# Kernel tuning notes

Measured on AMD Instinct MI355X. Metric: run time of the kernel, lower is better.

Reference implementation:

```python
import jax, jax.numpy as jnp
import numpy as np

N, E = 131072, 64
REL_SIZES = {0: (262144, 1), 1: (524288, 2), 2: (393216, 3)}  # idx_len, arity


def _mish(x):
    return x * jnp.tanh(jax.nn.softplus(x))


def _mlp(x, rw, rb, ow, ob):
    # torch MLP: output(input + mish(residual(input)))
    return (x + _mish(x @ rw + rb)) @ ow + ob


def setup_inputs() -> dict:
    key = jax.random.key(0)
    ks = jax.random.split(key, 16)

    def lin(k, fi, fo):
        k1, k2 = jax.random.split(k)
        lim = 1.0 / np.sqrt(fi)
        w = jax.random.uniform(k1, (fi, fo), jnp.float32, -lim, lim)
        b = jax.random.uniform(k2, (fo,), jnp.float32, -lim, lim)
        return w, b

    inp = {"obj_emb": jax.random.normal(ks[0], (N, E), jnp.float32)}
    for r in range(3):
        L, _ = REL_SIZES[r]
        inp[f"rel{r}_idx"] = jax.random.randint(ks[1 + r], (L,), 0, N, jnp.int64)
    for r in range(3):
        _, a = REL_SIZES[r]
        d = a * E
        w, b = lin(ks[4 + 2 * r], d, d)
        inp[f"r{r}_res_w"], inp[f"r{r}_res_b"] = w, b
        w, b = lin(ks[5 + 2 * r], d, d)
        inp[f"r{r}_out_w"], inp[f"r{r}_out_b"] = w, b
    w, b = lin(ks[10], 2 * E, 2 * E)
    inp["upd_res_w"], inp["upd_res_b"] = w, b
    w, b = lin(ks[11], 2 * E, E)
    inp["upd_out_w"], inp["upd_out_b"] = w, b
    return inp


def _forward(obj_emb, idxs, rel_params, upd_params):
    n, e = obj_emb.shape
    outs = []
    for (idx, a), (rw, rb, ow, ob) in zip(idxs, rel_params):
        g = obj_emb[idx].reshape(-1, a * e)          # gather -> [T, a*E]
        outs.append((idx, _mlp(g, rw, rb, ow, ob).reshape(-1, e)))
    # First scatter_reduce_('amax', include_self=False): positions written by
    # relation 0 ignore the initial 0; all other positions keep/compete with 0.
    written0 = jnp.zeros((n,), bool).at[idxs[0][0]].set(True)
    m = jnp.broadcast_to(jnp.where(written0[:, None], -jnp.inf, 0.0).astype(obj_emb.dtype), (n, e))
    for idx, out in outs:
        m = m.at[idx].max(out)
    m = jax.lax.stop_gradient(m)
    s = jnp.full((n, e), 1e-16, obj_emb.dtype)
    for idx, out in outs:
        s = s.at[idx].add(jnp.exp(12.0 * (out - m[idx])))
    max_msg = jnp.log(s) / 12.0 + m
    return _mlp(jnp.concatenate([max_msg, obj_emb], axis=1), *upd_params)


def reference(obj_emb, rel0_idx, rel1_idx, rel2_idx,
              r0_res_w, r0_res_b, r0_out_w, r0_out_b,
              r1_res_w, r1_res_b, r1_out_w, r1_out_b,
              r2_res_w, r2_res_b, r2_out_w, r2_out_b,
              upd_res_w, upd_res_b, upd_out_w, upd_out_b):
    idxs = [(rel0_idx, 1), (rel1_idx, 2), (rel2_idx, 3)]
    rel_params = [
        (r0_res_w, r0_res_b, r0_out_w, r0_out_b),
        (r1_res_w, r1_res_b, r1_out_w, r1_out_b),
        (r2_res_w, r2_res_b, r2_out_w, r2_out_b),
    ]
    return _forward(obj_emb, idxs, rel_params,
                    (upd_res_w, upd_res_b, upd_out_w, upd_out_b))
```

## Files before the change

kernel.cpp:

```cpp
#include <hip/hip_runtime.h>
#include <stdint.h>

typedef unsigned short u16;
typedef __bf16 bf16x8 __attribute__((ext_vector_type(8)));
typedef float floatx4 __attribute__((ext_vector_type(4)));

#define N_OBJ    131072
#define L0R      262144
#define L1R      524288
#define L2R      393216
#define TOTI     (L0R + L1R + L2R)


__device__ __forceinline__ float bf2f(u16 u) {
  union { uint32_t i; float f; } v; v.i = ((uint32_t)u) << 16; return v.f;
}
__device__ __forceinline__ u16 f2bf(float f) {
  union { float f; uint32_t i; } v; v.f = f;
  uint32_t r = (v.i + 0x7FFFu + ((v.i >> 16) & 1u)) >> 16;
  return (u16)r;
}
__device__ __forceinline__ uint4 pack8(const float* sp) {
  float4 f0 = *(const float4*)(sp);
  float4 f1 = *(const float4*)(sp + 4);
  uint4 v;
  v.x = (uint32_t)f2bf(f0.x) | ((uint32_t)f2bf(f0.y) << 16);
  v.y = (uint32_t)f2bf(f0.z) | ((uint32_t)f2bf(f0.w) << 16);
  v.z = (uint32_t)f2bf(f1.x) | ((uint32_t)f2bf(f1.y) << 16);
  v.w = (uint32_t)f2bf(f1.z) | ((uint32_t)f2bf(f1.w) << 16);
  return v;
}
__device__ __forceinline__ float mish_f(float x) {
  float t = __expf(fminf(x, 30.f));
  float u = 1.f + t; u = u * u;
  return x * (u - 1.f) / (u + 1.f);
}

__global__ __launch_bounds__(256) void norm_kernel(
    const int* __restrict__ r0, const int* __restrict__ r1,
    const int* __restrict__ r2, int* __restrict__ n)
{
  int g = blockIdx.x * 256 + (int)threadIdx.x;
  const int* src; int off;
  if (g < L0R)              { src = r0; off = g; }
  else if (g < L0R + L1R)   { src = r1; off = g - L0R; }
  else                      { src = r2; off = g - L0R - L1R; }
  int lane = (int)threadIdx.x & 63;
  int probe = src[2 * lane + 1];
  bool i64 = (__ballot(probe == 0) == ~0ull);
  n[g] = i64 ? src[2 * off] : src[off];
}

__global__ __launch_bounds__(256) void prep_kernel(
    const float* w0, const float* w1, const float* w2, const float* w3,
    const float* w4, const float* w5, const float* w6, const float* w7,
    u16* __restrict__ wt)
{
  int b = blockIdx.x;
  const float* srcs[8] = {w0, w1, w2, w3, w4, w5, w6, w7};
  const int fi[8]   = {64, 64, 128, 128, 192, 192, 128, 128};
  const int fo[8]   = {64, 64, 128, 128, 192, 192, 128, 64};
  const int boff[9] = {0, 16, 32, 96, 160, 304, 448, 512, 544};
  const int woff[8] = {0, 4096, 8192, 24576, 40960, 77824, 114688, 131072};
  int m = 0;
  #pragma unroll
  for (int j = 0; j < 8; ++j) if (b >= boff[j + 1]) m = j + 1;
  int e = (b - boff[m]) * 256 + (int)threadIdx.x;
  int k = e / fo[m];
  int n = e - k * fo[m];
  wt[woff[m] + n * fi[m] + k] = f2bf(srcs[m][e]);
}

__global__ __launch_bounds__(256) void flag_kernel(
    const int* __restrict__ idx0, unsigned char* __restrict__ flag)
{
  int g = blockIdx.x * 256 + (int)threadIdx.x;
  flag[idx0[g]] = 1;
}

template<int D, int NTOUT>
__device__ __forceinline__ void matmul_phase(
    const u16* __restrict__ wtsrc, u16* w_lds,
    const bf16x8 (&af)[D / 32], floatx4 (&acc)[D / 16],
    int tid, int q, int i)
{
  constexpr int PITCH = D + 8;
  #pragma unroll
  for (int t = 0; t < NTOUT; ++t) acc[t] = (floatx4)0.f;
  #pragma unroll
  for (int ch = 0; ch < NTOUT / 4; ++ch) {
    __syncthreads();
    for (int c = tid; c < 64 * (D / 8); c += 256) {
      int nr = c / (D / 8), p = c - nr * (D / 8);
      *(uint4*)(&w_lds[nr * PITCH + p * 8]) =
          *(const uint4*)(wtsrc + (size_t)(ch * 64 + nr) * D + p * 8);
    }
    __syncthreads();
    #pragma unroll
    for (int k = 0; k < D / 32; ++k) {
      #pragma unroll
      for (int nt = 0; nt < 4; ++nt) {
        bf16x8 bf = *(const bf16x8*)(&w_lds[(nt * 16 + i) * PITCH + k * 32 + q * 8]);
        acc[ch * 4 + nt] =
            __builtin_amdgcn_mfma_f32_16x16x32_bf16(af[k], bf, acc[ch * 4 + nt], 0, 0, 0);
      }
    }
  }
}

template<int D, int DOUT, int MODE>
__global__ __launch_bounds__(256, (D >= 192) ? 3 : 4) void mlp_kernel(
    const float* __restrict__ srcE, const u16* __restrict__ srcM,
    const int* __restrict__ idx,
    const u16* __restrict__ rwt, const float* __restrict__ rb,
    const u16* __restrict__ owt, const float* __restrict__ ob,
    float* __restrict__ dstF, float* __restrict__ dstS)
{
  constexpr int A = D / 64;
  constexpr int PITCH = D + 8;
  constexpr int NT1 = D / 16;
  constexpr int NT2 = DOUT / 16;
  constexpr int KI = D / 32;
  __shared__ alignas(16) u16 g_lds[64 * PITCH];
  __shared__ alignas(16) u16 w_lds[64 * PITCH];
  __shared__ float b1_lds[D];
  __shared__ float b2_lds[DOUT];
  __shared__ int i_lds[64 * A];

  const int tid = threadIdx.x;
  const int wave = tid >> 6;
  const int lane = tid & 63;
  const int q = lane >> 4;
  const int i = lane & 15;
  const int t0 = blockIdx.x * 64;

  for (int c = tid; c < D; c += 256) b1_lds[c] = rb[c];
  for (int c = tid; c < DOUT; c += 256) b2_lds[c] = ob[c];
  if (MODE == 0 && tid < 64 * A) i_lds[tid] = idx[t0 * A + tid];

  for (int c = tid; c < 64 * A * 8; c += 256) {
    int e = c >> 3, p = c & 7;
    int r = e / A, sl = e - r * A;
    uint4 val;
    if (MODE == 0) {
      int obj = idx[(t0 + r) * A + sl];
      val = pack8(srcE + (size_t)obj * 64 + p * 8);
    } else {
      if (sl == 0) val = *(const uint4*)(srcM + (size_t)(t0 + r) * 64 + p * 8);
      else         val = pack8(srcE + (size_t)(t0 + r) * 64 + p * 8);
    }
    *(uint4*)(&g_lds[r * PITCH + sl * 64 + p * 8]) = val;
  }
  __syncthreads();

  floatx4 acc[NT1];
  bf16x8 af[KI];

  #pragma unroll
  for (int k = 0; k < KI; ++k)
    af[k] = *(const bf16x8*)(&g_lds[(wave * 16 + i) * PITCH + k * 32 + q * 8]);
  matmul_phase<D, NT1>(rwt, w_lds, af, acc, tid, q, i);

  #pragma unroll
  for (int t = 0; t < NT1; ++t) {
    #pragma unroll
    for (int r = 0; r < 4; ++r) {
      int row = wave * 16 + q * 4 + r;
      int col = t * 16 + i;
      float h = acc[t][r] + b1_lds[col];
      float g = bf2f(g_lds[row * PITCH + col]);
      g_lds[row * PITCH + col] = f2bf(g + mish_f(h));
    }
  }

  #pragma unroll
  for (int k = 0; k < KI; ++k)
    af[k] = *(const bf16x8*)(&g_lds[(wave * 16 + i) * PITCH + k * 32 + q * 8]);
  matmul_phase<D, NT2>(owt, w_lds, af, acc, tid, q, i);

  #pragma unroll
  for (int t = 0; t < NT2; ++t) {
    #pragma unroll
    for (int r = 0; r < 4; ++r) {
      int row = wave * 16 + q * 4 + r;
      int col = t * 16 + i;
      float y = acc[t][r] + b2_lds[col];
      if (MODE == 0) {
        int slot = col >> 6, cc = col & 63;
        int obj = i_lds[row * A + slot];
        atomicAdd(&dstS[(size_t)obj * 64 + cc], __expf(fminf(12.f * y, 82.f)));
      } else {
        dstF[(size_t)(t0 + row) * 64 + col] = y;
      }
    }
  }
}

__global__ __launch_bounds__(256) void final_kernel(
    const float* __restrict__ s, const unsigned char* __restrict__ flag,
    u16* __restrict__ maxmsg)
{
  int tid = (int)threadIdx.x;
  int o = blockIdx.x * 64 + (tid >> 2);
  int c0 = (tid & 3) * 16;
  float add = flag[o] ? 1e-37f : 1e-16f;
  const float* sp = s + (size_t)o * 64 + c0;
  u16* mp = maxmsg + (size_t)o * 64 + c0;
  u16 tmp[16];
  #pragma unroll
  for (int j = 0; j < 16; ++j)
    tmp[j] = f2bf(__logf(sp[j] + add) * (1.f / 12.f));
  *(uint4*)(mp)     = *(uint4*)(tmp);
  *(uint4*)(mp + 8) = *(uint4*)(tmp + 8);
}

extern "C" void kernel_launch(void* const* d_in, const int* in_sizes, int n_in,
                              void* d_out, int out_size, void* d_ws, size_t ws_size,
                              hipStream_t stream)
{
  (void)in_sizes; (void)n_in; (void)out_size; (void)ws_size;
  const float* obj_emb = (const float*)d_in[0];
  const float* r0rb = (const float*)d_in[5];
  const float* r0ob = (const float*)d_in[7];
  const float* r1rb = (const float*)d_in[9];
  const float* r1ob = (const float*)d_in[11];
  const float* r2rb = (const float*)d_in[13];
  const float* r2ob = (const float*)d_in[15];
  const float* urb  = (const float*)d_in[17];
  const float* uob  = (const float*)d_in[19];

  char* ws = (char*)d_ws;
  float* s           = (float*)(ws);
  u16* wt            = (u16*)(ws + 33554432ull);
  unsigned char* flg = (unsigned char*)(ws + 33832960ull);
  u16* maxmsg        = (u16*)(ws + 33964032ull);
  int* nidx          = (int*)(ws + 50741248ull);
  float* out         = (float*)d_out;

  hipMemsetAsync(s, 0, 64ull * N_OBJ * 4ull, stream);
  hipMemsetAsync(flg, 0, N_OBJ, stream);

  norm_kernel<<<TOTI / 256, 256, 0, stream>>>(
      (const int*)d_in[1], (const int*)d_in[2], (const int*)d_in[3], nidx);
  prep_kernel<<<544, 256, 0, stream>>>(
      (const float*)d_in[4], (const float*)d_in[6], (const float*)d_in[8],
      (const float*)d_in[10], (const float*)d_in[12], (const float*)d_in[14],
      (const float*)d_in[16], (const float*)d_in[18], wt);
  flag_kernel<<<L0R / 256, 256, 0, stream>>>(nidx, flg);

  mlp_kernel<64, 64, 0><<<4096, 256, 0, stream>>>(
      obj_emb, nullptr, nidx, wt + 0, r0rb, wt + 4096, r0ob, nullptr, s);
  mlp_kernel<128, 128, 0><<<4096, 256, 0, stream>>>(
      obj_emb, nullptr, nidx + L0R, wt + 8192, r1rb, wt + 24576, r1ob, nullptr, s);
  mlp_kernel<192, 192, 0><<<2048, 256, 0, stream>>>(
      obj_emb, nullptr, nidx + L0R + L1R, wt + 40960, r2rb, wt + 77824, r2ob, nullptr, s);

  final_kernel<<<N_OBJ / 64, 256, 0, stream>>>(s, flg, maxmsg);

  mlp_kernel<128, 64, 1><<<2048, 256, 0, stream>>>(
      obj_emb, maxmsg, nullptr, wt + 114688, urb, wt + 131072, uob, out, nullptr);
}
```

Baseline: 482.4 us.

## Accumulate softmax sums in bf16 with packed atomic adds

The exp-sum accumulator moves from fp32 to bf16. Adjacent lanes pair their values through a shuffle so that a single global_atomic_pk_add_bf16 updates two columns at once, and the final kernel reads the bf16 sums with vector loads. This halves the accumulator footprint and the memset size, and halves the number of atomic operations, which targets the scatter-atomic bottleneck. The cost is accumulation precision: summing many exp terms in bf16 loses accuracy and may exceed the tolerance.

```diff
diff --git a/kernel.cpp b/kernel.cpp
--- a/kernel.cpp
+++ b/kernel.cpp
@@ -114,7 +114,7 @@
     const int* __restrict__ idx,
     const u16* __restrict__ rwt, const float* __restrict__ rb,
     const u16* __restrict__ owt, const float* __restrict__ ob,
-    float* __restrict__ dstF, float* __restrict__ dstS)
+    float* __restrict__ dstF, u16* __restrict__ dstS)
 {
   constexpr int A = D / 64;
   constexpr int PITCH = D + 8;
@@ -178,38 +178,63 @@
     af[k] = *(const bf16x8*)(&g_lds[(wave * 16 + i) * PITCH + k * 32 + q * 8]);
   matmul_phase<D, NT2>(owt, w_lds, af, acc, tid, q, i);
 
-  #pragma unroll
-  for (int t = 0; t < NT2; ++t) {
-    #pragma unroll
-    for (int r = 0; r < 4; ++r) {
-      int row = wave * 16 + q * 4 + r;
+  if (MODE == 0) {
+    #pragma unroll
+    for (int t = 0; t < NT2; ++t) {
       int col = t * 16 + i;
-      float y = acc[t][r] + b2_lds[col];
-      if (MODE == 0) {
-        int slot = col >> 6, cc = col & 63;
-        int obj = i_lds[row * A + slot];
-        atomicAdd(&dstS[(size_t)obj * 64 + cc], __expf(fminf(12.f * y, 82.f)));
-      } else {
-        dstF[(size_t)(t0 + row) * 64 + col] = y;
+      int slot = col >> 6, cc = col & 63;
+      float e[4], p[4];
+      #pragma unroll
+      for (int r = 0; r < 4; ++r)
+        e[r] = __expf(fminf(12.f * (acc[t][r] + b2_lds[col]), 82.f));
+      #pragma unroll
+      for (int r = 0; r < 4; ++r) p[r] = __shfl_xor(e[r], 1);
+      if ((i & 1) == 0) {
+        #pragma unroll
+        for (int r = 0; r < 4; ++r) {
+          int row = wave * 16 + q * 4 + r;
+          int obj = i_lds[row * A + slot];
+          uint32_t packed = (uint32_t)f2bf(e[r]) | ((uint32_t)f2bf(p[r]) << 16);
+          u16* addr = dstS + (size_t)obj * 64 + cc;
+          asm volatile("global_atomic_pk_add_bf16 %0, %1, off"
+                       :: "v"(addr), "v"(packed) : "memory");
+        }
       }
     }
+    asm volatile("s_waitcnt vmcnt(0)" ::: "memory");
+  } else {
+    #pragma unroll
+    for (int t = 0; t < NT2; ++t) {
+      #pragma unroll
+      for (int r = 0; r < 4; ++r) {
+        int row = wave * 16 + q * 4 + r;
+        int col = t * 16 + i;
+        dstF[(size_t)(t0 + row) * 64 + col] = acc[t][r] + b2_lds[col];
+      }
+    }
   }
 }
 
 __global__ __launch_bounds__(256) void final_kernel(
-    const float* __restrict__ s, const unsigned char* __restrict__ flag,
+    const u16* __restrict__ s, const unsigned char* __restrict__ flag,
     u16* __restrict__ maxmsg)
 {
   int tid = (int)threadIdx.x;
   int o = blockIdx.x * 64 + (tid >> 2);
   int c0 = (tid & 3) * 16;
   float add = flag[o] ? 1e-37f : 1e-16f;
-  const float* sp = s + (size_t)o * 64 + c0;
+  const u16* sp = s + (size_t)o * 64 + c0;
   u16* mp = maxmsg + (size_t)o * 64 + c0;
+  union { uint4 v; u16 a[8]; } in0, in1;
+  in0.v = *(const uint4*)(sp);
+  in1.v = *(const uint4*)(sp + 8);
   u16 tmp[16];
   #pragma unroll
-  for (int j = 0; j < 16; ++j)
-    tmp[j] = f2bf(__logf(sp[j] + add) * (1.f / 12.f));
+  for (int j = 0; j < 8; ++j)
+    tmp[j] = f2bf(__logf(bf2f(in0.a[j]) + add) * (1.f / 12.f));
+  #pragma unroll
+  for (int j = 0; j < 8; ++j)
+    tmp[8 + j] = f2bf(__logf(bf2f(in1.a[j]) + add) * (1.f / 12.f));
   *(uint4*)(mp)     = *(uint4*)(tmp);
   *(uint4*)(mp + 8) = *(uint4*)(tmp + 8);
 }
@@ -230,14 +255,14 @@
   const float* uob  = (const float*)d_in[19];
 
   char* ws = (char*)d_ws;
-  float* s           = (float*)(ws);
-  u16* wt            = (u16*)(ws + 33554432ull);
-  unsigned char* flg = (unsigned char*)(ws + 33832960ull);
-  u16* maxmsg        = (u16*)(ws + 33964032ull);
-  int* nidx          = (int*)(ws + 50741248ull);
+  u16* s             = (u16*)(ws);
+  u16* wt            = (u16*)(ws + 16777216ull);
+  unsigned char* flg = (unsigned char*)(ws + 17055744ull);
+  u16* maxmsg        = (u16*)(ws + 17186816ull);
+  int* nidx          = (int*)(ws + 33964032ull);
   float* out         = (float*)d_out;
 
-  hipMemsetAsync(s, 0, 64ull * N_OBJ * 4ull, stream);
+  hipMemsetAsync(s, 0, 64ull * N_OBJ * 2ull, stream);
   hipMemsetAsync(flg, 0, N_OBJ, stream);
 
   norm_kernel<<<TOTI / 256, 256, 0, stream>>>(
```

Measured after the change: 480.3 us. No clear change (-0.4%).

## Replace atomic scatter-add with CSR bucketing and segmented per-object reduction

Applied to the files above, without the earlier changes.

The float atomicAdd scatter of exp(12*y) messages into a per-object accumulator is replaced with a CSR-style plan. Per-object degrees are counted during index normalisation and turned into offsets by a three-kernel prefix scan. The relation MLPs then claim a slot with a per-index cursor atomic and write bf16 exp messages there, and a new reduce kernel sums each object's contiguous segment with one wave per object before taking the log. This trades the many contended float atomics for a large bf16 message buffer write and read plus the scan kernels. It also rounds each term to bf16 before summation. The new path runs only if the workspace holds about 175 MB; otherwise the old atomic path is used.

```diff
diff --git a/kernel.cpp b/kernel.cpp
--- a/kernel.cpp
+++ b/kernel.cpp
@@ -38,7 +38,7 @@
 
 __global__ __launch_bounds__(256) void norm_kernel(
     const int* __restrict__ r0, const int* __restrict__ r1,
-    const int* __restrict__ r2, int* __restrict__ n)
+    const int* __restrict__ r2, int* __restrict__ n, int* __restrict__ cnt)
 {
   int g = blockIdx.x * 256 + (int)threadIdx.x;
   const int* src; int off;
@@ -48,7 +48,9 @@
   int lane = (int)threadIdx.x & 63;
   int probe = src[2 * lane + 1];
   bool i64 = (__ballot(probe == 0) == ~0ull);
-  n[g] = i64 ? src[2 * off] : src[off];
+  int v = i64 ? src[2 * off] : src[off];
+  n[g] = v;
+  if (cnt) atomicAdd(&cnt[v], 1);
 }
 
 __global__ __launch_bounds__(256) void prep_kernel(
@@ -76,6 +78,54 @@
 {
   int g = blockIdx.x * 256 + (int)threadIdx.x;
   flag[idx0[g]] = 1;
+}
+
+__global__ __launch_bounds__(256) void scan_a(
+    const int* __restrict__ count, int* __restrict__ thrpre,
+    int* __restrict__ blocksum)
+{
+  int tid = (int)threadIdx.x, b = blockIdx.x;
+  int o = b * 1024 + tid * 4;
+  int t = count[o] + count[o + 1] + count[o + 2] + count[o + 3];
+  __shared__ int sd[256];
+  sd[tid] = t; __syncthreads();
+  for (int off = 1; off < 256; off <<= 1) {
+    int v = (tid >= off) ? sd[tid - off] : 0;
+    __syncthreads();
+    sd[tid] += v;
+    __syncthreads();
+  }
+  thrpre[b * 256 + tid] = sd[tid] - t;
+  if (tid == 255) blocksum[b] = sd[tid];
+}
+__global__ __launch_bounds__(128) void scan_b(int* __restrict__ blocksum)
+{
+  int tid = (int)threadIdx.x;
+  int t = blocksum[tid];
+  __shared__ int sd[128];
+  sd[tid] = t; __syncthreads();
+  for (int off = 1; off < 128; off <<= 1) {
+    int v = (tid >= off) ? sd[tid - off] : 0;
+    __syncthreads();
+    sd[tid] += v;
+    __syncthreads();
+  }
+  blocksum[tid] = sd[tid] - t;
+}
+__global__ __launch_bounds__(256) void scan_c(
+    const int* __restrict__ count, const int* __restrict__ thrpre,
+    const int* __restrict__ blocksum, int* __restrict__ offsets,
+    int* __restrict__ cursor)
+{
+  int tid = (int)threadIdx.x, b = blockIdx.x;
+  int o = b * 1024 + tid * 4;
+  int base = blocksum[b] + thrpre[b * 256 + tid];
+  #pragma unroll
+  for (int j = 0; j < 4; ++j) {
+    offsets[o + j] = base;
+    cursor[o + j] = base;
+    base += count[o + j];
+  }
 }
 
 template<int D, int NTOUT>
@@ -114,7 +164,8 @@
     const int* __restrict__ idx,
     const u16* __restrict__ rwt, const float* __restrict__ rb,
     const u16* __restrict__ owt, const float* __restrict__ ob,
-    float* __restrict__ dstF, float* __restrict__ dstS)
+    float* __restrict__ dstF, float* __restrict__ sAt,
+    u16* __restrict__ msg, int* __restrict__ cursor)
 {
   constexpr int A = D / 64;
   constexpr int PITCH = D + 8;
@@ -126,6 +177,7 @@
   __shared__ float b1_lds[D];
   __shared__ float b2_lds[DOUT];
   __shared__ int i_lds[64 * A];
+  __shared__ int p_lds[64 * A];
 
   const int tid = threadIdx.x;
   const int wave = tid >> 6;
@@ -136,13 +188,17 @@
 
   for (int c = tid; c < D; c += 256) b1_lds[c] = rb[c];
   for (int c = tid; c < DOUT; c += 256) b2_lds[c] = ob[c];
-  if (MODE == 0 && tid < 64 * A) i_lds[tid] = idx[t0 * A + tid];
+  if (MODE != 1 && tid < 64 * A) {
+    int obj = idx[t0 * A + tid];
+    i_lds[tid] = obj;
+    if (MODE == 0) p_lds[tid] = atomicAdd(&cursor[obj], 1);
+  }
 
   for (int c = tid; c < 64 * A * 8; c += 256) {
     int e = c >> 3, p = c & 7;
     int r = e / A, sl = e - r * A;
     uint4 val;
-    if (MODE == 0) {
+    if (MODE != 1) {
       int obj = idx[(t0 + r) * A + sl];
       val = pack8(srcE + (size_t)obj * 64 + p * 8);
     } else {
@@ -187,13 +243,33 @@
       float y = acc[t][r] + b2_lds[col];
       if (MODE == 0) {
         int slot = col >> 6, cc = col & 63;
+        float e = __expf(fminf(12.f * y, 82.f));
+        int pos = p_lds[row * A + slot];
+        msg[(size_t)pos * 64 + cc] = f2bf(e);
+      } else if (MODE == 2) {
+        int slot = col >> 6, cc = col & 63;
         int obj = i_lds[row * A + slot];
-        atomicAdd(&dstS[(size_t)obj * 64 + cc], __expf(fminf(12.f * y, 82.f)));
+        atomicAdd(&sAt[(size_t)obj * 64 + cc], __expf(fminf(12.f * y, 82.f)));
       } else {
         dstF[(size_t)(t0 + row) * 64 + col] = y;
       }
     }
   }
+}
+
+__global__ __launch_bounds__(256) void reduce_kernel(
+    const u16* __restrict__ msg, const int* __restrict__ count,
+    const int* __restrict__ offsets, const unsigned char* __restrict__ flag,
+    u16* __restrict__ maxmsg)
+{
+  int wv = (int)threadIdx.x >> 6, lane = (int)threadIdx.x & 63;
+  int o = blockIdx.x * 4 + wv;
+  int deg = count[o], start = offsets[o];
+  const u16* mp = msg + (size_t)start * 64 + lane;
+  float s = 0.f;
+  for (int j = 0; j < deg; ++j) s += bf2f(mp[(size_t)j * 64]);
+  float add = flag[o] ? 1e-37f : 1e-16f;
+  maxmsg[(size_t)o * 64 + lane] = f2bf(__logf(s + add) * (1.f / 12.f));
 }
 
 __global__ __launch_bounds__(256) void final_kernel(
@@ -218,7 +294,7 @@
                               void* d_out, int out_size, void* d_ws, size_t ws_size,
                               hipStream_t stream)
 {
-  (void)in_sizes; (void)n_in; (void)out_size; (void)ws_size;
+  (void)in_sizes; (void)n_in; (void)out_size;
   const float* obj_emb = (const float*)d_in[0];
   const float* r0rb = (const float*)d_in[5];
   const float* r0ob = (const float*)d_in[7];
@@ -228,35 +304,83 @@
   const float* r2ob = (const float*)d_in[15];
   const float* urb  = (const float*)d_in[17];
   const float* uob  = (const float*)d_in[19];
-
+  float* out = (float*)d_out;
   char* ws = (char*)d_ws;
-  float* s           = (float*)(ws);
-  u16* wt            = (u16*)(ws + 33554432ull);
-  unsigned char* flg = (unsigned char*)(ws + 33832960ull);
-  u16* maxmsg        = (u16*)(ws + 33964032ull);
-  int* nidx          = (int*)(ws + 50741248ull);
-  float* out         = (float*)d_out;
-
-  hipMemsetAsync(s, 0, 64ull * N_OBJ * 4ull, stream);
-  hipMemsetAsync(flg, 0, N_OBJ, stream);
-
-  norm_kernel<<<TOTI / 256, 256, 0, stream>>>(
-      (const int*)d_in[1], (const int*)d_in[2], (const int*)d_in[3], nidx);
-  prep_kernel<<<544, 256, 0, stream>>>(
-      (const float*)d_in[4], (const float*)d_in[6], (const float*)d_in[8],
-      (const float*)d_in[10], (const float*)d_in[12], (const float*)d_in[14],
-      (const float*)d_in[16], (const float*)d_in[18], wt);
-  flag_kernel<<<L0R / 256, 256, 0, stream>>>(nidx, flg);
-
-  mlp_kernel<64, 64, 0><<<4096, 256, 0, stream>>>(
-      obj_emb, nullptr, nidx, wt + 0, r0rb, wt + 4096, r0ob, nullptr, s);
-  mlp_kernel<128, 128, 0><<<4096, 256, 0, stream>>>(
-      obj_emb, nullptr, nidx + L0R, wt + 8192, r1rb, wt + 24576, r1ob, nullptr, s);
-  mlp_kernel<192, 192, 0><<<2048, 256, 0, stream>>>(
-      obj_emb, nullptr, nidx + L0R + L1R, wt + 40960, r2rb, wt + 77824, r2ob, nullptr, s);
-
-  final_kernel<<<N_OBJ / 64, 256, 0, stream>>>(s, flg, maxmsg);
-
-  mlp_kernel<128, 64, 1><<<2048, 256, 0, stream>>>(
-      obj_emb, maxmsg, nullptr, wt + 114688, urb, wt + 131072, uob, out, nullptr);
-}
+
+  const size_t NEED = 174605312ull;
+  if (ws_size >= NEED) {
+    u16* msg           = (u16*)(ws);
+    u16* wt            = (u16*)(ws + 150994944ull);
+    unsigned char* flg = (unsigned char*)(ws + 151273472ull);
+    u16* maxmsg        = (u16*)(ws + 151404544ull);
+    int* nidx          = (int*)(ws + 168181760ull);
+    int* count         = (int*)(ws + 172900352ull);
+    int* offsets       = (int*)(ws + 173424640ull);
+    int* cursor        = (int*)(ws + 173948928ull);
+    int* thrpre        = (int*)(ws + 174473216ull);
+    int* blocksum      = (int*)(ws + 174604288ull);
+
+    hipMemsetAsync(count, 0, N_OBJ * 4, stream);
+    hipMemsetAsync(flg, 0, N_OBJ, stream);
+
+    norm_kernel<<<TOTI / 256, 256, 0, stream>>>(
+        (const int*)d_in[1], (const int*)d_in[2], (const int*)d_in[3], nidx, count);
+    prep_kernel<<<544, 256, 0, stream>>>(
+        (const float*)d_in[4], (const float*)d_in[6], (const float*)d_in[8],
+        (const float*)d_in[10], (const float*)d_in[12], (const float*)d_in[14],
+        (const float*)d_in[16], (const float*)d_in[18], wt);
+    flag_kernel<<<L0R / 256, 256, 0, stream>>>(nidx, flg);
+    scan_a<<<128, 256, 0, stream>>>(count, thrpre, blocksum);
+    scan_b<<<1, 128, 0, stream>>>(blocksum);
+    scan_c<<<128, 256, 0, stream>>>(count, thrpre, blocksum, offsets, cursor);
+
+    mlp_kernel<64, 64, 0><<<4096, 256, 0, stream>>>(
+        obj_emb, nullptr, nidx, wt + 0, r0rb, wt + 4096, r0ob,
+        nullptr, nullptr, msg, cursor);
+    mlp_kernel<128, 128, 0><<<4096, 256, 0, stream>>>(
+        obj_emb, nullptr, nidx + L0R, wt + 8192, r1rb, wt + 24576, r1ob,
+        nullptr, nullptr, msg, cursor);
+    mlp_kernel<192, 192, 0><<<2048, 256, 0, stream>>>(
+        obj_emb, nullptr, nidx + L0R + L1R, wt + 40960, r2rb, wt + 77824, r2ob,
+        nullptr, nullptr, msg, cursor);
+
+    reduce_kernel<<<N_OBJ / 4, 256, 0, stream>>>(msg, count, offsets, flg, maxmsg);
+
+    mlp_kernel<128, 64, 1><<<2048, 256, 0, stream>>>(
+        obj_emb, maxmsg, nullptr, wt + 114688, urb, wt + 131072, uob,
+        out, nullptr, nullptr, nullptr);
+  } else {
+    float* s           = (float*)(ws);
+    u16* wt            = (u16*)(ws + 33554432ull);
+    unsigned char* flg = (unsigned char*)(ws + 33832960ull);
+    u16* maxmsg        = (u16*)(ws + 33964032ull);
+    int* nidx          = (int*)(ws + 50741248ull);
+
+    hipMemsetAsync(s, 0, 64ull * N_OBJ * 4ull, stream);
+    hipMemsetAsync(flg, 0, N_OBJ, stream);
+
+    norm_kernel<<<TOTI / 256, 256, 0, stream>>>(
+        (const int*)d_in[1], (const int*)d_in[2], (const int*)d_in[3], nidx, nullptr);
+    prep_kernel<<<544, 256, 0, stream>>>(
+        (const float*)d_in[4], (const float*)d_in[6], (const float*)d_in[8],
+        (const float*)d_in[10], (const float*)d_in[12], (const float*)d_in[14],
+        (const float*)d_in[16], (const float*)d_in[18], wt);
+    flag_kernel<<<L0R / 256, 256, 0, stream>>>(nidx, flg);
+
+    mlp_kernel<64, 64, 2><<<4096, 256, 0, stream>>>(
+        obj_emb, nullptr, nidx, wt + 0, r0rb, wt + 4096, r0ob,
+        nullptr, s, nullptr, nullptr);
+    mlp_kernel<128, 128, 2><<<4096, 256, 0, stream>>>(
+        obj_emb, nullptr, nidx + L0R, wt + 8192, r1rb, wt + 24576, r1ob,
+        nullptr, s, nullptr, nullptr);
+    mlp_kernel<192, 192, 2><<<2048, 256, 0, stream>>>(
+        obj_emb, nullptr, nidx + L0R + L1R, wt + 40960, r2rb, wt + 77824, r2ob,
+        nullptr, s, nullptr, nullptr);
+
+    final_kernel<<<N_OBJ / 64, 256, 0, stream>>>(s, flg, maxmsg);
+
+    mlp_kernel<128, 64, 1><<<2048, 256, 0, stream>>>(
+        obj_emb, maxmsg, nullptr, wt + 114688, urb, wt + 131072, uob,
+        out, nullptr, nullptr, nullptr);
+  }
+}
```

After: 496.9 us. 1.03x slower.
